# Kernel optimization log

Measured on AMD Instinct MI355X. Metric: run time of the kernel, lower is better.

Reference implementation:

```python
import jax, jax.numpy as jnp
import numpy as np

B, T, H = 32, 512, 1024

def setup_inputs() -> dict:
    key = jax.random.key(0)
    k1, k2, k3, k4, k5 = jax.random.split(key, 5)
    s = 1.0 / np.sqrt(H)  # torch LSTM init scale
    return {
        "x": jax.random.normal(k1, (B, T, H), dtype=jnp.float32),
        "w_ih": jax.random.uniform(k2, (4 * H, H), jnp.float32, -s, s),
        "w_hh": jax.random.uniform(k3, (4 * H, H), jnp.float32, -s, s),
        "b_ih": jax.random.uniform(k4, (4 * H,), jnp.float32, -s, s),
        "b_hh": jax.random.uniform(k5, (4 * H,), jnp.float32, -s, s),
    }

def reference(x, w_ih, w_hh, b_ih, b_hh):
    # Precompute input projections for all steps: [T, B, 4H]
    xg = jnp.einsum('bth,gh->tbg', x, w_ih) + b_ih + b_hh
    h0 = jnp.zeros((x.shape[0], H), x.dtype)
    c0 = jnp.zeros_like(h0)

    def step(carry, xg_t):
        h, c = carry
        gates = xg_t + h @ w_hh.T            # [B, 4H]
        i, f, g, o = jnp.split(gates, 4, axis=-1)  # torch order: i,f,g,o
        i = jax.nn.sigmoid(i)
        f = jax.nn.sigmoid(f)
        g = jnp.tanh(g)
        o = jax.nn.sigmoid(o)
        c = f * c + i * g
        h = o * jnp.tanh(c)
        return (h, c), None

    (h_n, _), _ = jax.lax.scan(step, (h0, c0), xg)
    return h_n  # [B, H] == h_n[0] in torch
```

## Files before the change

### kernel.cpp

```cpp
#include <hip/hip_runtime.h>
#include <cmath>

#define Tn 512
#define Bn 32
#define Hn 1024

typedef short bf16x8 __attribute__((ext_vector_type(8)));
typedef float f32x4 __attribute__((ext_vector_type(4)));

__device__ __forceinline__ unsigned short f2bf_rne(float f) {
    unsigned u = __float_as_uint(f);
    unsigned r = (u + 0x7fffu + ((u >> 16) & 1u)) >> 16;
    return (unsigned short)r;
}
__device__ __forceinline__ float bf2f(unsigned short h) {
    return __uint_as_float((unsigned)h << 16);
}
__device__ __forceinline__ bf16x8 cvt8(float4 a, float4 b) {
    union { unsigned u[4]; bf16x8 v; } o;
    o.u[0] = (unsigned)f2bf_rne(a.x) | ((unsigned)f2bf_rne(a.y) << 16);
    o.u[1] = (unsigned)f2bf_rne(a.z) | ((unsigned)f2bf_rne(a.w) << 16);
    o.u[2] = (unsigned)f2bf_rne(b.x) | ((unsigned)f2bf_rne(b.y) << 16);
    o.u[3] = (unsigned)f2bf_rne(b.z) | ((unsigned)f2bf_rne(b.w) << 16);
    return o.v;
}
__device__ __forceinline__ bf16x8 as_bf8(uint4 u) {
    union { uint4 q; bf16x8 v; } o; o.q = u; return o.v;
}

__device__ __forceinline__ float fsigf(float x) {
    return __builtin_amdgcn_rcpf(1.f + __expf(-x));
}
__device__ __forceinline__ float ftanhf(float x) {
    return 1.f - 2.f * __builtin_amdgcn_rcpf(1.f + __expf(2.f * x));
}

__device__ __forceinline__ void gstore_u32_sc(unsigned* p, unsigned v) {
    asm volatile("global_store_dword %0, %1, off sc0 sc1\n\t"
                 "s_waitcnt vmcnt(0)"
                 :: "v"(p), "v"(v) : "memory");
}
__device__ __forceinline__ void gstore_u32_nd(unsigned* p, unsigned v) {
    asm volatile("global_store_dword %0, %1, off sc0 sc1"
                 :: "v"(p), "v"(v) : "memory");
}
__device__ __forceinline__ unsigned gload_u32_sc(const unsigned* p) {
    unsigned r;
    asm volatile("global_load_dword %0, %1, off sc0 sc1\n\t"
                 "s_waitcnt vmcnt(0)"
                 : "=&v"(r) : "v"(p) : "memory");
    return r;
}
__device__ __forceinline__ void gload_h_sc(const unsigned short* b0,
                                           const unsigned short* b1,
                                           uint4* o0, uint4* o1) {
    asm volatile(
        "global_load_dwordx4 %0, %8, off sc0 sc1\n\t"
        "global_load_dwordx4 %1, %8, off offset:64 sc0 sc1\n\t"
        "global_load_dwordx4 %2, %8, off offset:128 sc0 sc1\n\t"
        "global_load_dwordx4 %3, %8, off offset:192 sc0 sc1\n\t"
        "global_load_dwordx4 %4, %9, off sc0 sc1\n\t"
        "global_load_dwordx4 %5, %9, off offset:64 sc0 sc1\n\t"
        "global_load_dwordx4 %6, %9, off offset:128 sc0 sc1\n\t"
        "global_load_dwordx4 %7, %9, off offset:192 sc0 sc1\n\t"
        "s_waitcnt vmcnt(0)"
        : "=&v"(o0[0]), "=&v"(o0[1]), "=&v"(o0[2]), "=&v"(o0[3]),
          "=&v"(o1[0]), "=&v"(o1[1]), "=&v"(o1[2]), "=&v"(o1[3])
        : "v"(b0), "v"(b1)
        : "memory");
}

__global__ void lstm_flags_init(unsigned* flags) { flags[threadIdx.x] = 0u; }

__global__ __launch_bounds__(512, 2) void lstm_persist_mfma(
    const float* __restrict__ x,
    const float* __restrict__ w_ih,
    const float* __restrict__ w_hh,
    const float* __restrict__ b_ih,
    const float* __restrict__ b_hh,
    unsigned short* __restrict__ hbuf,
    unsigned* __restrict__ flags,
    float* __restrict__ out)
{
    extern __shared__ char smem[];
    unsigned short* lds_w = (unsigned short*)smem;
    float* lds_r = (float*)(smem + 131584);
    unsigned* lds_cnt = (unsigned*)(smem + 131584 + 16384);

    const int tid = threadIdx.x;
    const int bj  = blockIdx.x;
    const int wv  = tid >> 6;
    const int ln  = tid & 63;
    const int l15 = ln & 15;
    const int qd  = ln >> 4;

    if (tid == 0) *lds_cnt = 0u;

    for (int i = 0; i < 16; ++i) {
        int slot = i * 512 + tid;
        int r    = slot >> 9;
        int f4   = slot & 511;
        int n    = (r >> 2) * Hn + bj * 4 + (r & 3);
        float4 v = (f4 < 256) ? ((const float4*)(w_ih + (size_t)n * Hn))[f4]
                              : ((const float4*)(w_hh + (size_t)n * Hn))[f4 - 256];
        unsigned short h0 = f2bf_rne(v.x), h1 = f2bf_rne(v.y);
        unsigned short h2 = f2bf_rne(v.z), h3 = f2bf_rne(v.w);
        unsigned short l0 = f2bf_rne(v.x - bf2f(h0)), l1 = f2bf_rne(v.y - bf2f(h1));
        unsigned short l2 = f2bf_rne(v.z - bf2f(h2)), l3 = f2bf_rne(v.w - bf2f(h3));
        uint2 ph, pl;
        ph.x = (unsigned)h0 | ((unsigned)h1 << 16);
        ph.y = (unsigned)h2 | ((unsigned)h3 << 16);
        pl.x = (unsigned)l0 | ((unsigned)l1 << 16);
        pl.y = (unsigned)l2 | ((unsigned)l3 << 16);
        *(uint2*)(lds_w + (size_t)r        * 2056 + f4 * 4) = ph;
        *(uint2*)(lds_w + (size_t)(r + 16) * 2056 + f4 * 4) = pl;
    }

    float bias0 = 0.f, bias1 = 0.f, bias2 = 0.f, bias3 = 0.f, creg = 0.f;
    if (ln < 16) {
        int col = bj * 4 + (ln & 3);
        bias0 = b_ih[col]          + b_hh[col];
        bias1 = b_ih[Hn + col]     + b_hh[Hn + col];
        bias2 = b_ih[2 * Hn + col] + b_hh[2 * Hn + col];
        bias3 = b_ih[3 * Hn + col] + b_hh[3 * Hn + col];
    }
    __syncthreads();

    const unsigned short* whi_base = lds_w + (size_t)l15 * 2056 + qd * 8;
    const unsigned short* wlo_base = lds_w + (size_t)(l15 + 16) * 2056 + qd * 8;
    const float* xr0 = x + (size_t)l15        * (Tn * Hn) + wv * 128 + qd * 8;
    const float* xr1 = x + (size_t)(16 + l15) * (Tn * Hn) + wv * 128 + qd * 8;
    const size_t hoff0 = (size_t)l15        * Hn + wv * 128 + qd * 8;
    const size_t hoff1 = (size_t)(16 + l15) * Hn + wv * 128 + qd * 8;

    float4 xa0[4], xb0[4], xa1[4], xb1[4];
    #pragma unroll
    for (int j = 0; j < 4; ++j) {
        xa0[j] = *(const float4*)(xr0 + j * 32);
        xb0[j] = *(const float4*)(xr0 + j * 32 + 4);
        xa1[j] = *(const float4*)(xr1 + j * 32);
        xb1[j] = *(const float4*)(xr1 + j * 32 + 4);
    }

    for (int t = 0; t < Tn; ++t) {
        f32x4 a0h = {0.f,0.f,0.f,0.f}, a0l = {0.f,0.f,0.f,0.f};
        f32x4 a1h = {0.f,0.f,0.f,0.f}, a1l = {0.f,0.f,0.f,0.f};

        float4 na0[4], nb0[4], na1[4], nb1[4];
        {
            const int tn = (t + 1 < Tn) ? (t + 1) : t;
            const float* p0 = xr0 + (size_t)tn * Hn;
            const float* p1 = xr1 + (size_t)tn * Hn;
            #pragma unroll
            for (int j = 0; j < 4; ++j) {
                na0[j] = *(const float4*)(p0 + j * 32);
                nb0[j] = *(const float4*)(p0 + j * 32 + 4);
                na1[j] = *(const float4*)(p1 + j * 32);
                nb1[j] = *(const float4*)(p1 + j * 32 + 4);
            }
        }

        #pragma unroll
        for (int j = 0; j < 4; ++j) {
            const int koff = wv * 128 + j * 32;
            bf16x8 ahi = *(const bf16x8*)(whi_base + koff);
            bf16x8 alo = *(const bf16x8*)(wlo_base + koff);
            bf16x8 bf0 = cvt8(xa0[j], xb0[j]);
            bf16x8 bf1 = cvt8(xa1[j], xb1[j]);
            a0h = __builtin_amdgcn_mfma_f32_16x16x32_bf16(ahi, bf0, a0h, 0, 0, 0);
            a0l = __builtin_amdgcn_mfma_f32_16x16x32_bf16(alo, bf0, a0l, 0, 0, 0);
            a1h = __builtin_amdgcn_mfma_f32_16x16x32_bf16(ahi, bf1, a1h, 0, 0, 0);
            a1l = __builtin_amdgcn_mfma_f32_16x16x32_bf16(alo, bf1, a1l, 0, 0, 0);
        }

        if (t > 0) {
            {
                const int src = (ln < 32) ? (wv * 32 + ln) : bj;
                const unsigned* fp = flags + src;
                bool done = false;
                for (;;) {
                    if (!done) done = (gload_u32_sc(fp) >= (unsigned)t);
                    if (__all((int)done)) break;
                }
            }
            const unsigned short* hb = hbuf + (size_t)((t - 1) & 1) * (Bn * Hn);
            uint4 hf0[4], hf1[4];
            gload_h_sc(hb + hoff0, hb + hoff1, hf0, hf1);
            #pragma unroll
            for (int j = 0; j < 4; ++j) {
                const int koff = 1024 + wv * 128 + j * 32;
                bf16x8 ahi = *(const bf16x8*)(whi_base + koff);
                bf16x8 alo = *(const bf16x8*)(wlo_base + koff);
                bf16x8 bf0 = as_bf8(hf0[j]);
                bf16x8 bf1 = as_bf8(hf1[j]);
                a0h = __builtin_amdgcn_mfma_f32_16x16x32_bf16(ahi, bf0, a0h, 0, 0, 0);
                a0l = __builtin_amdgcn_mfma_f32_16x16x32_bf16(alo, bf0, a0l, 0, 0, 0);
                a1h = __builtin_amdgcn_mfma_f32_16x16x32_bf16(ahi, bf1, a1h, 0, 0, 0);
                a1l = __builtin_amdgcn_mfma_f32_16x16x32_bf16(alo, bf1, a1l, 0, 0, 0);
            }
        }

        {
            f32x4 acc0 = a0h + a0l;
            f32x4 acc1 = a1h + a1l;
            float* pr0 = lds_r + (wv * 2 + 0) * 256 + l15;
            float* pr1 = lds_r + (wv * 2 + 1) * 256 + l15;
            #pragma unroll
            for (int r = 0; r < 4; ++r) {
                pr0[(qd * 4 + r) * 16] = acc0[r];
                pr1[(qd * 4 + r) * 16] = acc1[r];
            }
        }
        __syncthreads();

        if (ln < 16) {
            const int e   = (wv << 4) | ln;
            const int b   = e >> 2;
            const int cl  = e & 3;
            const int bt  = b >> 4, c16 = b & 15;
            float s0 = 0.f, s1 = 0.f, s2 = 0.f, s3 = 0.f;
            #pragma unroll
            for (int w8 = 0; w8 < 8; ++w8) {
                const float* base = lds_r + (w8 * 2 + bt) * 256 + c16;
                s0 += base[(0 * 4 + cl) * 16];
                s1 += base[(1 * 4 + cl) * 16];
                s2 += base[(2 * 4 + cl) * 16];
                s3 += base[(3 * 4 + cl) * 16];
            }
            float iv = fsigf(s0 + bias0);
            float fv = fsigf(s1 + bias1);
            float gv = ftanhf(s2 + bias2);
            float ov = fsigf(s3 + bias3);
            creg = fv * creg + iv * gv;
            float hn = ov * ftanhf(creg);
            unsigned short hv = f2bf_rne(hn);
            unsigned up = (unsigned)__shfl_xor((int)(unsigned)hv, 1, 64);
            if (!(ln & 1)) {
                unsigned pack = (unsigned)hv | (up << 16);
                unsigned short* hw = hbuf + (size_t)(t & 1) * (Bn * Hn)
                                   + (size_t)b * Hn + bj * 4 + cl;
                gstore_u32_nd((unsigned*)hw, pack);
            }
            if (t == Tn - 1) out[(size_t)b * Hn + bj * 4 + cl] = hn;
        }
        asm volatile("s_waitcnt vmcnt(0)" ::: "memory");
        if (ln == 0) {
            unsigned old = atomicAdd(lds_cnt, 1u);
            if (old == 8u * (unsigned)t + 7u && (t + 1 < Tn))
                gstore_u32_sc(&flags[bj], (unsigned)(t + 1));
        }

        #pragma unroll
        for (int j = 0; j < 4; ++j) {
            xa0[j] = na0[j]; xb0[j] = nb0[j];
            xa1[j] = na1[j]; xb1[j] = nb1[j];
        }
    }
}

extern "C" void kernel_launch(void* const* d_in, const int* in_sizes, int n_in,
                              void* d_out, int out_size, void* d_ws, size_t ws_size,
                              hipStream_t stream) {
    const float* x    = (const float*)d_in[0];
    const float* w_ih = (const float*)d_in[1];
    const float* w_hh = (const float*)d_in[2];
    const float* b_ih = (const float*)d_in[3];
    const float* b_hh = (const float*)d_in[4];
    float* out = (float*)d_out;

    char* ws = (char*)d_ws;
    unsigned*       flags = (unsigned*)ws;
    unsigned short* hbuf  = (unsigned short*)(ws + 1024);
    (void)in_sizes; (void)n_in; (void)out_size; (void)ws_size;

    const size_t smem_bytes = 131584 + 16384 + 16;

    lstm_flags_init<<<dim3(1), dim3(256), 0, stream>>>(flags);
    lstm_persist_mfma<<<dim3(256), dim3(512), smem_bytes, stream>>>(
        x, w_ih, w_hh, b_ih, b_hh, hbuf, flags, out);
}
```

Before: 3.909 ms.

## Split input projection into chunked GEMM kernel ahead of recurrent persistent kernel

Removes the x·W_ih contribution from the serial recurrent loop and computes it in a separate MFMA GEMM kernel over chunks of 64 timesteps, writing xg to workspace. The persistent kernel now keeps only W_hh in LDS, which halves its LDS footprint, and reads the precomputed gate inputs each step. Cell state is carried across chunk launches through a global cbuf. The cost is 16 extra kernel launches, persistent-kernel restarts that reload weights each chunk, and extra global traffic for xg. The W_ih GEMM is also recomputed per block tile with LDS staging.

Measured after the change: 4.369 ms. +11.8%, slower.

```diff
diff --git a/kernel.cpp b/kernel.cpp
--- a/kernel.cpp
+++ b/kernel.cpp
@@ -4,6 +4,7 @@
 #define Tn 512
 #define Bn 32
 #define Hn 1024
+#define CH 64
 
 typedef short bf16x8 __attribute__((ext_vector_type(8)));
 typedef float f32x4 __attribute__((ext_vector_type(4)));
@@ -72,20 +73,109 @@
 
 __global__ void lstm_flags_init(unsigned* flags) { flags[threadIdx.x] = 0u; }
 
-__global__ __launch_bounds__(512, 2) void lstm_persist_mfma(
+__global__ __launch_bounds__(512, 2) void lstm_xg_gemm(
     const float* __restrict__ x,
     const float* __restrict__ w_ih,
+    float* __restrict__ xg,
+    int t0)
+{
+    extern __shared__ char smem[];
+    unsigned short* lds_a = (unsigned short*)smem;
+
+    const int tid = threadIdx.x;
+    const int gct = blockIdx.x & 31;
+    const int tt  = blockIdx.x >> 5;
+    const int wv  = tid >> 6;
+    const int ln  = tid & 63;
+    const int l15 = ln & 15;
+    const int qd  = ln >> 4;
+    const int tl  = tt * 8 + wv;
+    const int tg  = t0 + tl;
+
+    f32x4 acc[8][2];
+    #pragma unroll
+    for (int gs = 0; gs < 8; ++gs)
+        #pragma unroll
+        for (int h2 = 0; h2 < 2; ++h2)
+            acc[gs][h2] = (f32x4){0.f, 0.f, 0.f, 0.f};
+
+    const float* xrow0 = x + (size_t)l15 * (Tn * Hn) + (size_t)tg * Hn + qd * 8;
+    const float* xrow1 = xrow0 + (size_t)16 * (Tn * Hn);
+
+    for (int kt = 0; kt < 8; ++kt) {
+        #pragma unroll
+        for (int it = 0; it < 8; ++it) {
+            int fi  = it * 512 + tid;
+            int row = fi >> 5;
+            int c   = fi & 31;
+            float4 v = *(const float4*)(w_ih + (size_t)(gct * 128 + row) * Hn
+                                        + kt * 128 + c * 4);
+            unsigned short h0 = f2bf_rne(v.x), h1 = f2bf_rne(v.y);
+            unsigned short h2 = f2bf_rne(v.z), h3 = f2bf_rne(v.w);
+            unsigned short u0 = f2bf_rne(v.x - bf2f(h0)), u1 = f2bf_rne(v.y - bf2f(h1));
+            unsigned short u2 = f2bf_rne(v.z - bf2f(h2)), u3 = f2bf_rne(v.w - bf2f(h3));
+            uint2 ph, pl;
+            ph.x = (unsigned)h0 | ((unsigned)h1 << 16);
+            ph.y = (unsigned)h2 | ((unsigned)h3 << 16);
+            pl.x = (unsigned)u0 | ((unsigned)u1 << 16);
+            pl.y = (unsigned)u2 | ((unsigned)u3 << 16);
+            *(uint2*)(lds_a + (size_t)row * 136 + c * 4) = ph;
+            *(uint2*)(lds_a + (size_t)(row + 128) * 136 + c * 4) = pl;
+        }
+        __syncthreads();
+
+        float4 xv[4][4];
+        #pragma unroll
+        for (int kk = 0; kk < 4; ++kk) {
+            xv[kk][0] = *(const float4*)(xrow0 + kt * 128 + kk * 32);
+            xv[kk][1] = *(const float4*)(xrow0 + kt * 128 + kk * 32 + 4);
+            xv[kk][2] = *(const float4*)(xrow1 + kt * 128 + kk * 32);
+            xv[kk][3] = *(const float4*)(xrow1 + kt * 128 + kk * 32 + 4);
+        }
+        #pragma unroll
+        for (int kk = 0; kk < 4; ++kk) {
+            bf16x8 bf0 = cvt8(xv[kk][0], xv[kk][1]);
+            bf16x8 bf1 = cvt8(xv[kk][2], xv[kk][3]);
+            #pragma unroll
+            for (int gs = 0; gs < 8; ++gs) {
+                bf16x8 ahi = *(const bf16x8*)(lds_a + (size_t)(gs * 16 + l15) * 136
+                                              + kk * 32 + qd * 8);
+                bf16x8 alo = *(const bf16x8*)(lds_a + (size_t)(128 + gs * 16 + l15) * 136
+                                              + kk * 32 + qd * 8);
+                acc[gs][0] = __builtin_amdgcn_mfma_f32_16x16x32_bf16(ahi, bf0, acc[gs][0], 0, 0, 0);
+                acc[gs][0] = __builtin_amdgcn_mfma_f32_16x16x32_bf16(alo, bf0, acc[gs][0], 0, 0, 0);
+                acc[gs][1] = __builtin_amdgcn_mfma_f32_16x16x32_bf16(ahi, bf1, acc[gs][1], 0, 0, 0);
+                acc[gs][1] = __builtin_amdgcn_mfma_f32_16x16x32_bf16(alo, bf1, acc[gs][1], 0, 0, 0);
+            }
+        }
+        __syncthreads();
+    }
+
+    float* xgp = xg + (size_t)tl * (4096 * 32) + (size_t)(gct * 128) * 32 + l15;
+    #pragma unroll
+    for (int gs = 0; gs < 8; ++gs)
+        #pragma unroll
+        for (int h2 = 0; h2 < 2; ++h2)
+            #pragma unroll
+            for (int r = 0; r < 4; ++r)
+                xgp[(size_t)(gs * 16 + qd * 4 + r) * 32 + h2 * 16] = acc[gs][h2][r];
+}
+
+__global__ __launch_bounds__(512, 2) void lstm_persist_mfma(
     const float* __restrict__ w_hh,
     const float* __restrict__ b_ih,
     const float* __restrict__ b_hh,
+    const float* __restrict__ xg,
     unsigned short* __restrict__ hbuf,
+    float* __restrict__ cbuf,
     unsigned* __restrict__ flags,
-    float* __restrict__ out)
+    float* __restrict__ out,
+    int t0)
 {
     extern __shared__ char smem[];
     unsigned short* lds_w = (unsigned short*)smem;
-    float* lds_r = (float*)(smem + 131584);
-    unsigned* lds_cnt = (unsigned*)(smem + 131584 + 16384);
+    float* lds_r = (float*)(smem + 66048);
+    unsigned* lds_cnt = (unsigned*)(smem + 66048 + 18432);
 
     const int tid = threadIdx.x;
     const int bj  = blockIdx.x;
@@ -96,82 +186,58 @@
 
     if (tid == 0) *lds_cnt = 0u;
 
-    for (int i = 0; i < 16; ++i) {
+    for (int i = 0; i < 8; ++i) {
         int slot = i * 512 + tid;
-        int r    = slot >> 9;
-        int f4   = slot & 511;
+        int r    = slot >> 8;
+        int f4   = slot & 255;
         int n    = (r >> 2) * Hn + bj * 4 + (r & 3);
-        float4 v = (f4 < 256) ? ((const float4*)(w_ih + (size_t)n * Hn))[f4]
-                              : ((const float4*)(w_hh + (size_t)n * Hn))[f4 - 256];
+        float4 v = ((const float4*)(w_hh + (size_t)n * Hn))[f4];
         unsigned short h0 = f2bf_rne(v.x), h1 = f2bf_rne(v.y);
         unsigned short h2 = f2bf_rne(v.z), h3 = f2bf_rne(v.w);
-        unsigned short l0 = f2bf_rne(v.x - bf2f(h0)), l1 = f2bf_rne(v.y - bf2f(h1));
-        unsigned short l2 = f2bf_rne(v.z - bf2f(h2)), l3 = f2bf_rne(v.w - bf2f(h3));
+        unsigned short u0 = f2bf_rne(v.x - bf2f(h0)), u1 = f2bf_rne(v.y - bf2f(h1));
+        unsigned short u2 = f2bf_rne(v.z - bf2f(h2)), u3 = f2bf_rne(v.w - bf2f(h3));
         uint2 ph, pl;
         ph.x = (unsigned)h0 | ((unsigned)h1 << 16);
         ph.y = (unsigned)h2 | ((unsigned)h3 << 16);
-        pl.x = (unsigned)l0 | ((unsigned)l1 << 16);
-        pl.y = (unsigned)l2 | ((unsigned)l3 << 16);
-        *(uint2*)(lds_w + (size_t)r        * 2056 + f4 * 4) = ph;
-        *(uint2*)(lds_w + (size_t)(r + 16) * 2056 + f4 * 4) = pl;
+        pl.x = (unsigned)u0 | ((unsigned)u1 << 16);
+        pl.y = (unsigned)u2 | ((unsigned)u3 << 16);
+        *(uint2*)(lds_w + (size_t)r        * 1032 + f4 * 4) = ph;
+        *(uint2*)(lds_w + (size_t)(r + 16) * 1032 + f4 * 4) = pl;
     }
 
     float bias0 = 0.f, bias1 = 0.f, bias2 = 0.f, bias3 = 0.f, creg = 0.f;
+    int fb = 0, fcl = 0;
     if (ln < 16) {
-        int col = bj * 4 + (ln & 3);
+        const int e = (wv << 4) | ln;
+        fb  = e >> 2;
+        fcl = e & 3;
+        int col = bj * 4 + fcl;
         bias0 = b_ih[col]          + b_hh[col];
         bias1 = b_ih[Hn + col]     + b_hh[Hn + col];
         bias2 = b_ih[2 * Hn + col] + b_hh[2 * Hn + col];
         bias3 = b_ih[3 * Hn + col] + b_hh[3 * Hn + col];
+        if (t0 > 0) creg = cbuf[(size_t)fb * Hn + col];
     }
     __syncthreads();
 
-    const unsigned short* whi_base = lds_w + (size_t)l15 * 2056 + qd * 8;
-    const unsigned short* wlo_base = lds_w + (size_t)(l15 + 16) * 2056 + qd * 8;
-    const float* xr0 = x + (size_t)l15        * (Tn * Hn) + wv * 128 + qd * 8;
-    const float* xr1 = x + (size_t)(16 + l15) * (Tn * Hn) + wv * 128 + qd * 8;
+    const unsigned short* whi_base = lds_w + (size_t)l15 * 1032 + qd * 8;
+    const unsigned short* wlo_base = lds_w + (size_t)(l15 + 16) * 1032 + qd * 8;
     const size_t hoff0 = (size_t)l15        * Hn + wv * 128 + qd * 8;
     const size_t hoff1 = (size_t)(16 + l15) * Hn + wv * 128 + qd * 8;
 
-    float4 xa0[4], xb0[4], xa1[4], xb1[4];
-    #pragma unroll
-    for (int j = 0; j < 4; ++j) {
-        xa0[j] = *(const float4*)(xr0 + j * 32);
-        xb0[j] = *(const float4*)(xr0 + j * 32 + 4);
-        xa1[j] = *(const float4*)(xr1 + j * 32);
-        xb1[j] = *(const float4*)(xr1 + j * 32 + 4);
-    }
-
-    for (int t = 0; t < Tn; ++t) {
+    for (int t = t0; t < t0 + CH; ++t) {
+        float xg0 = 0.f, xg1 = 0.f, xg2 = 0.f, xg3 = 0.f;
+        if (ln < 16) {
+            const float* xp = xg + (size_t)(t - t0) * (4096 * 32)
+                            + (size_t)(bj * 4 + fcl) * 32 + fb;
+            xg0 = xp[0];
+            xg1 = xp[1 * 1024 * 32];
+            xg2 = xp[2 * 1024 * 32];
+            xg3 = xp[3 * 1024 * 32];
+        }
+
         f32x4 a0h = {0.f,0.f,0.f,0.f}, a0l = {0.f,0.f,0.f,0.f};
         f32x4 a1h = {0.f,0.f,0.f,0.f}, a1l = {0.f,0.f,0.f,0.f};
-
-        float4 na0[4], nb0[4], na1[4], nb1[4];
-        {
-            const int tn = (t + 1 < Tn) ? (t + 1) : t;
-            const float* p0 = xr0 + (size_t)tn * Hn;
-            const float* p1 = xr1 + (size_t)tn * Hn;
-            #pragma unroll
-            for (int j = 0; j < 4; ++j) {
-                na0[j] = *(const float4*)(p0 + j * 32);
-                nb0[j] = *(const float4*)(p0 + j * 32 + 4);
-                na1[j] = *(const float4*)(p1 + j * 32);
-                nb1[j] = *(const float4*)(p1 + j * 32 + 4);
-            }
-        }
-
-        #pragma unroll
-        for (int j = 0; j < 4; ++j) {
-            const int koff = wv * 128 + j * 32;
-            bf16x8 ahi = *(const bf16x8*)(whi_base + koff);
-            bf16x8 alo = *(const bf16x8*)(wlo_base + koff);
-            bf16x8 bf0 = cvt8(xa0[j], xb0[j]);
-            bf16x8 bf1 = cvt8(xa1[j], xb1[j]);
-            a0h = __builtin_amdgcn_mfma_f32_16x16x32_bf16(ahi, bf0, a0h, 0, 0, 0);
-            a0l = __builtin_amdgcn_mfma_f32_16x16x32_bf16(alo, bf0, a0l, 0, 0, 0);
-            a1h = __builtin_amdgcn_mfma_f32_16x16x32_bf16(ahi, bf1, a1h, 0, 0, 0);
-            a1l = __builtin_amdgcn_mfma_f32_16x16x32_bf16(alo, bf1, a1l, 0, 0, 0);
-        }
 
         if (t > 0) {
             {
@@ -188,7 +254,7 @@
             gload_h_sc(hb + hoff0, hb + hoff1, hf0, hf1);
             #pragma unroll
             for (int j = 0; j < 4; ++j) {
-                const int koff = 1024 + wv * 128 + j * 32;
+                const int koff = wv * 128 + j * 32;
                 bf16x8 ahi = *(const bf16x8*)(whi_base + koff);
                 bf16x8 alo = *(const bf16x8*)(wlo_base + koff);
                 bf16x8 bf0 = as_bf8(hf0[j]);
@@ -203,34 +269,31 @@
         {
             f32x4 acc0 = a0h + a0l;
             f32x4 acc1 = a1h + a1l;
-            float* pr0 = lds_r + (wv * 2 + 0) * 256 + l15;
-            float* pr1 = lds_r + (wv * 2 + 1) * 256 + l15;
+            float* pr0 = lds_r + (wv * 2 + 0) * 288 + l15;
+            float* pr1 = lds_r + (wv * 2 + 1) * 288 + l15;
             #pragma unroll
             for (int r = 0; r < 4; ++r) {
-                pr0[(qd * 4 + r) * 16] = acc0[r];
-                pr1[(qd * 4 + r) * 16] = acc1[r];
+                pr0[(qd * 4 + r) * 18] = acc0[r];
+                pr1[(qd * 4 + r) * 18] = acc1[r];
             }
         }
         __syncthreads();
 
         if (ln < 16) {
-            const int e   = (wv << 4) | ln;
-            const int b   = e >> 2;
-            const int cl  = e & 3;
-            const int bt  = b >> 4, c16 = b & 15;
+            const int bt = fb >> 4, c16 = fb & 15;
             float s0 = 0.f, s1 = 0.f, s2 = 0.f, s3 = 0.f;
             #pragma unroll
             for (int w8 = 0; w8 < 8; ++w8) {
-                const float* base = lds_r + (w8 * 2 + bt) * 256 + c16;
-                s0 += base[(0 * 4 + cl) * 16];
-                s1 += base[(1 * 4 + cl) * 16];
-                s2 += base[(2 * 4 + cl) * 16];
-                s3 += base[(3 * 4 + cl) * 16];
-            }
-            float iv = fsigf(s0 + bias0);
-            float fv = fsigf(s1 + bias1);
-            float gv = ftanhf(s2 + bias2);
-            float ov = fsigf(s3 + bias3);
+                const float* base = lds_r + (w8 * 2 + bt) * 288 + c16;
+                s0 += base[(0 * 4 + fcl) * 18];
+                s1 += base[(1 * 4 + fcl) * 18];
+                s2 += base[(2 * 4 + fcl) * 18];
+                s3 += base[(3 * 4 + fcl) * 18];
+            }
+            float iv = fsigf(s0 + xg0 + bias0);
+            float fv = fsigf(s1 + xg1 + bias1);
+            float gv = ftanhf(s2 + xg2 + bias2);
+            float ov = fsigf(s3 + xg3 + bias3);
             creg = fv * creg + iv * gv;
             float hn = ov * ftanhf(creg);
             unsigned short hv = f2bf_rne(hn);
@@ -238,22 +301,18 @@
             if (!(ln & 1)) {
                 unsigned pack = (unsigned)hv | (up << 16);
                 unsigned short* hw = hbuf + (size_t)(t & 1) * (Bn * Hn)
-                                   + (size_t)b * Hn + bj * 4 + cl;
+                                   + (size_t)fb * Hn + bj * 4 + fcl;
                 gstore_u32_nd((unsigned*)hw, pack);
             }
-            if (t == Tn - 1) out[(size_t)b * Hn + bj * 4 + cl] = hn;
+            if (t == Tn - 1) out[(size_t)fb * Hn + bj * 4 + fcl] = hn;
+            if (t == t0 + CH - 1) cbuf[(size_t)fb * Hn + bj * 4 + fcl] = creg;
         }
         asm volatile("s_waitcnt vmcnt(0)" ::: "memory");
         if (ln == 0) {
+            unsigned lt = (unsigned)(t - t0);
             unsigned old = atomicAdd(lds_cnt, 1u);
-            if (old == 8u * (unsigned)t + 7u && (t + 1 < Tn))
+            if (old == 8u * lt + 7u && (t + 1 < Tn))
                 gstore_u32_sc(&flags[bj], (unsigned)(t + 1));
-        }
-
-        #pragma unroll
-        for (int j = 0; j < 4; ++j) {
-            xa0[j] = na0[j]; xb0[j] = nb0[j];
-            xa1[j] = na1[j]; xb1[j] = nb1[j];
         }
     }
 }
@@ -271,11 +330,18 @@
     char* ws = (char*)d_ws;
     unsigned*       flags = (unsigned*)ws;
     unsigned short* hbuf  = (unsigned short*)(ws + 1024);
+    float*          cbuf  = (float*)(ws + 1024 + 131072);
+    float*          xg    = (float*)(ws + 1024 + 131072 + 131072);
     (void)in_sizes; (void)n_in; (void)out_size; (void)ws_size;
 
-    const size_t smem_bytes = 131584 + 16384 + 16;
+    const size_t smem_a = 256 * 136 * 2;
+    const size_t smem_b = 66048 + 18432 + 16;
 
     lstm_flags_init<<<dim3(1), dim3(256), 0, stream>>>(flags);
-    lstm_persist_mfma<<<dim3(256), dim3(512), smem_bytes, stream>>>(
-        x, w_ih, w_hh, b_ih, b_hh, hbuf, flags, out);
-}
+    for (int c = 0; c < Tn / CH; ++c) {
+        lstm_xg_gemm<<<dim3(256), dim3(512), smem_a, stream>>>(
+            x, w_ih, xg, c * CH);
+        lstm_persist_mfma<<<dim3(256), dim3(512), smem_b, stream>>>(
+            w_hh, b_ih, b_hh, xg, hbuf, cbuf, flags, out, c * CH);
+    }
+}
```

## Restructure persistent LSTM into thin 2-wave blocks with per-half sync flags

Applied to the files above, without the earlier changes.

Each block now runs 2 waves instead of 8. Each wave owns 16 batch rows and covers the full K=1024 on its own, which removes the LDS cross-wave reduction and the __syncthreads on every step. The high part of W_hh is kept in registers, and the input projection for step t+1 runs after publishing h, so it overlaps with the wait. Flags are split per half and polled with vectorized min-of-4 loads plus s_sleep, and h is stored as 64-bit packs. In exchange, each wave now does serial per-step MFMA work over the whole K, and register pressure is very high with 32 bf16x8 weight registers plus 32 uint4 h loads.

Measured after the change: 10.78 ms. 176% more time.

```diff
diff --git a/kernel.cpp b/kernel.cpp
--- a/kernel.cpp
+++ b/kernel.cpp
@@ -40,39 +40,43 @@
                  "s_waitcnt vmcnt(0)"
                  :: "v"(p), "v"(v) : "memory");
 }
-__device__ __forceinline__ void gstore_u32_nd(unsigned* p, unsigned v) {
-    asm volatile("global_store_dword %0, %1, off sc0 sc1"
+__device__ __forceinline__ void gstore_u64_nd(unsigned long long* p,
+                                              unsigned long long v) {
+    asm volatile("global_store_dwordx2 %0, %1, off sc0 sc1"
                  :: "v"(p), "v"(v) : "memory");
 }
-__device__ __forceinline__ unsigned gload_u32_sc(const unsigned* p) {
-    unsigned r;
-    asm volatile("global_load_dword %0, %1, off sc0 sc1\n\t"
+__device__ __forceinline__ uint4 gload_u4_sc(const unsigned* p) {
+    uint4 r;
+    asm volatile("global_load_dwordx4 %0, %1, off sc0 sc1\n\t"
                  "s_waitcnt vmcnt(0)"
                  : "=&v"(r) : "v"(p) : "memory");
     return r;
 }
-__device__ __forceinline__ void gload_h_sc(const unsigned short* b0,
-                                           const unsigned short* b1,
-                                           uint4* o0, uint4* o1) {
+__device__ __forceinline__ void gload8_nd(const unsigned short* b, uint4* o) {
     asm volatile(
         "global_load_dwordx4 %0, %8, off sc0 sc1\n\t"
         "global_load_dwordx4 %1, %8, off offset:64 sc0 sc1\n\t"
         "global_load_dwordx4 %2, %8, off offset:128 sc0 sc1\n\t"
         "global_load_dwordx4 %3, %8, off offset:192 sc0 sc1\n\t"
-        "global_load_dwordx4 %4, %9, off sc0 sc1\n\t"
-        "global_load_dwordx4 %5, %9, off offset:64 sc0 sc1\n\t"
-        "global_load_dwordx4 %6, %9, off offset:128 sc0 sc1\n\t"
-        "global_load_dwordx4 %7, %9, off offset:192 sc0 sc1\n\t"
-        "s_waitcnt vmcnt(0)"
-        : "=&v"(o0[0]), "=&v"(o0[1]), "=&v"(o0[2]), "=&v"(o0[3]),
-          "=&v"(o1[0]), "=&v"(o1[1]), "=&v"(o1[2]), "=&v"(o1[3])
-        : "v"(b0), "v"(b1)
+        "global_load_dwordx4 %4, %8, off offset:256 sc0 sc1\n\t"
+        "global_load_dwordx4 %5, %8, off offset:320 sc0 sc1\n\t"
+        "global_load_dwordx4 %6, %8, off offset:384 sc0 sc1\n\t"
+        "global_load_dwordx4 %7, %8, off offset:448 sc0 sc1"
+        : "=&v"(o[0]), "=&v"(o[1]), "=&v"(o[2]), "=&v"(o[3]),
+          "=&v"(o[4]), "=&v"(o[5]), "=&v"(o[6]), "=&v"(o[7])
+        : "v"(b)
         : "memory");
 }
 
+__device__ __forceinline__ unsigned min4u(uint4 f) {
+    unsigned a = f.x < f.y ? f.x : f.y;
+    unsigned b = f.z < f.w ? f.z : f.w;
+    return a < b ? a : b;
+}
+
 __global__ void lstm_flags_init(unsigned* flags) { flags[threadIdx.x] = 0u; }
 
-__global__ __launch_bounds__(512, 2) void lstm_persist_mfma(
+__global__ __launch_bounds__(128, 1) void lstm_persist_thin(
     const float* __restrict__ x,
     const float* __restrict__ w_ih,
     const float* __restrict__ w_hh,
@@ -84,176 +88,164 @@
 {
     extern __shared__ char smem[];
     unsigned short* lds_w = (unsigned short*)smem;
-    float* lds_r = (float*)(smem + 131584);
-    unsigned* lds_cnt = (unsigned*)(smem + 131584 + 16384);
-
-    const int tid = threadIdx.x;
-    const int bj  = blockIdx.x;
-    const int wv  = tid >> 6;
-    const int ln  = tid & 63;
-    const int l15 = ln & 15;
-    const int qd  = ln >> 4;
-
-    if (tid == 0) *lds_cnt = 0u;
-
-    for (int i = 0; i < 16; ++i) {
-        int slot = i * 512 + tid;
-        int r    = slot >> 9;
-        int f4   = slot & 511;
-        int n    = (r >> 2) * Hn + bj * 4 + (r & 3);
-        float4 v = (f4 < 256) ? ((const float4*)(w_ih + (size_t)n * Hn))[f4]
-                              : ((const float4*)(w_hh + (size_t)n * Hn))[f4 - 256];
+
+    const int tid  = threadIdx.x;
+    const int bj   = blockIdx.x;
+    const int half = tid >> 6;
+    const int ln   = tid & 63;
+    const int l15  = ln & 15;
+    const int qd   = ln >> 4;
+
+    for (int i = 0; i < 64; ++i) {
+        int slot = i * 128 + tid;
+        int m    = slot >> 12;
+        int rr   = (slot >> 8) & 15;
+        int f4   = slot & 255;
+        const float* W = m ? w_hh : w_ih;
+        int n = (rr >> 2) * Hn + bj * 4 + (rr & 3);
+        float4 v = ((const float4*)(W + (size_t)n * Hn))[f4];
         unsigned short h0 = f2bf_rne(v.x), h1 = f2bf_rne(v.y);
         unsigned short h2 = f2bf_rne(v.z), h3 = f2bf_rne(v.w);
-        unsigned short l0 = f2bf_rne(v.x - bf2f(h0)), l1 = f2bf_rne(v.y - bf2f(h1));
-        unsigned short l2 = f2bf_rne(v.z - bf2f(h2)), l3 = f2bf_rne(v.w - bf2f(h3));
+        unsigned short u0 = f2bf_rne(v.x - bf2f(h0)), u1 = f2bf_rne(v.y - bf2f(h1));
+        unsigned short u2 = f2bf_rne(v.z - bf2f(h2)), u3 = f2bf_rne(v.w - bf2f(h3));
         uint2 ph, pl;
         ph.x = (unsigned)h0 | ((unsigned)h1 << 16);
         ph.y = (unsigned)h2 | ((unsigned)h3 << 16);
-        pl.x = (unsigned)l0 | ((unsigned)l1 << 16);
-        pl.y = (unsigned)l2 | ((unsigned)l3 << 16);
-        *(uint2*)(lds_w + (size_t)r        * 2056 + f4 * 4) = ph;
-        *(uint2*)(lds_w + (size_t)(r + 16) * 2056 + f4 * 4) = pl;
+        pl.x = (unsigned)u0 | ((unsigned)u1 << 16);
+        pl.y = (unsigned)u2 | ((unsigned)u3 << 16);
+        unsigned short* base = lds_w + (size_t)m * 33024;
+        *(uint2*)(base + (size_t)rr        * 1032 + f4 * 4) = ph;
+        *(uint2*)(base + (size_t)(rr + 16) * 1032 + f4 * 4) = pl;
     }
 
-    float bias0 = 0.f, bias1 = 0.f, bias2 = 0.f, bias3 = 0.f, creg = 0.f;
-    if (ln < 16) {
-        int col = bj * 4 + (ln & 3);
-        bias0 = b_ih[col]          + b_hh[col];
-        bias1 = b_ih[Hn + col]     + b_hh[Hn + col];
-        bias2 = b_ih[2 * Hn + col] + b_hh[2 * Hn + col];
-        bias3 = b_ih[3 * Hn + col] + b_hh[3 * Hn + col];
+    float bias[4];
+    {
+        int col = bj * 4 + qd;
+        #pragma unroll
+        for (int g = 0; g < 4; ++g)
+            bias[g] = b_ih[g * Hn + col] + b_hh[g * Hn + col];
     }
     __syncthreads();
 
-    const unsigned short* whi_base = lds_w + (size_t)l15 * 2056 + qd * 8;
-    const unsigned short* wlo_base = lds_w + (size_t)(l15 + 16) * 2056 + qd * 8;
-    const float* xr0 = x + (size_t)l15        * (Tn * Hn) + wv * 128 + qd * 8;
-    const float* xr1 = x + (size_t)(16 + l15) * (Tn * Hn) + wv * 128 + qd * 8;
-    const size_t hoff0 = (size_t)l15        * Hn + wv * 128 + qd * 8;
-    const size_t hoff1 = (size_t)(16 + l15) * Hn + wv * 128 + qd * 8;
-
-    float4 xa0[4], xb0[4], xa1[4], xb1[4];
+    const unsigned short* Axh = lds_w + (size_t)l15 * 1032 + qd * 8;
+    const unsigned short* Axl = Axh + (size_t)16 * 1032;
+    const unsigned short* Ahh = Axh + 33024;
+    const unsigned short* Ahl = Axl + 33024;
+    const float* xlane = x + (size_t)(half * 16 + l15) * (Tn * Hn) + qd * 8;
+    const size_t hlane = (size_t)(half * 16 + l15) * Hn + qd * 8;
+
+    bf16x8 whh[32];
     #pragma unroll
-    for (int j = 0; j < 4; ++j) {
-        xa0[j] = *(const float4*)(xr0 + j * 32);
-        xb0[j] = *(const float4*)(xr0 + j * 32 + 4);
-        xa1[j] = *(const float4*)(xr1 + j * 32);
-        xb1[j] = *(const float4*)(xr1 + j * 32 + 4);
-    }
+    for (int j = 0; j < 32; ++j)
+        whh[j] = *(const bf16x8*)(Ahh + j * 32);
+
+    f32x4 c0 = {0,0,0,0}, c1 = {0,0,0,0}, c2 = {0,0,0,0}, c3 = {0,0,0,0};
+    float creg = 0.f;
+
+    auto xphase = [&](int tt) {
+        const float* xp = xlane + (size_t)tt * Hn;
+        #pragma unroll
+        for (int jb = 0; jb < 4; ++jb) {
+            float4 va[8], vb[8];
+            #pragma unroll
+            for (int jj = 0; jj < 8; ++jj) {
+                va[jj] = *(const float4*)(xp + (jb * 8 + jj) * 32);
+                vb[jj] = *(const float4*)(xp + (jb * 8 + jj) * 32 + 4);
+            }
+            #pragma unroll
+            for (int jj = 0; jj < 8; ++jj) {
+                const int j = jb * 8 + jj;
+                bf16x8 xb  = cvt8(va[jj], vb[jj]);
+                bf16x8 ahi = *(const bf16x8*)(Axh + j * 32);
+                bf16x8 alo = *(const bf16x8*)(Axl + j * 32);
+                if (j & 1) {
+                    c2 = __builtin_amdgcn_mfma_f32_16x16x32_bf16(ahi, xb, c2, 0, 0, 0);
+                    c3 = __builtin_amdgcn_mfma_f32_16x16x32_bf16(alo, xb, c3, 0, 0, 0);
+                } else {
+                    c0 = __builtin_amdgcn_mfma_f32_16x16x32_bf16(ahi, xb, c0, 0, 0, 0);
+                    c1 = __builtin_amdgcn_mfma_f32_16x16x32_bf16(alo, xb, c1, 0, 0, 0);
+                }
+            }
+        }
+    };
+
+    xphase(0);
 
     for (int t = 0; t < Tn; ++t) {
-        f32x4 a0h = {0.f,0.f,0.f,0.f}, a0l = {0.f,0.f,0.f,0.f};
-        f32x4 a1h = {0.f,0.f,0.f,0.f}, a1l = {0.f,0.f,0.f,0.f};
-
-        float4 na0[4], nb0[4], na1[4], nb1[4];
-        {
-            const int tn = (t + 1 < Tn) ? (t + 1) : t;
-            const float* p0 = xr0 + (size_t)tn * Hn;
-            const float* p1 = xr1 + (size_t)tn * Hn;
-            #pragma unroll
-            for (int j = 0; j < 4; ++j) {
-                na0[j] = *(const float4*)(p0 + j * 32);
-                nb0[j] = *(const float4*)(p0 + j * 32 + 4);
-                na1[j] = *(const float4*)(p1 + j * 32);
-                nb1[j] = *(const float4*)(p1 + j * 32 + 4);
-            }
-        }
-
-        #pragma unroll
-        for (int j = 0; j < 4; ++j) {
-            const int koff = wv * 128 + j * 32;
-            bf16x8 ahi = *(const bf16x8*)(whi_base + koff);
-            bf16x8 alo = *(const bf16x8*)(wlo_base + koff);
-            bf16x8 bf0 = cvt8(xa0[j], xb0[j]);
-            bf16x8 bf1 = cvt8(xa1[j], xb1[j]);
-            a0h = __builtin_amdgcn_mfma_f32_16x16x32_bf16(ahi, bf0, a0h, 0, 0, 0);
-            a0l = __builtin_amdgcn_mfma_f32_16x16x32_bf16(alo, bf0, a0l, 0, 0, 0);
-            a1h = __builtin_amdgcn_mfma_f32_16x16x32_bf16(ahi, bf1, a1h, 0, 0, 0);
-            a1l = __builtin_amdgcn_mfma_f32_16x16x32_bf16(alo, bf1, a1l, 0, 0, 0);
-        }
-
         if (t > 0) {
             {
-                const int src = (ln < 32) ? (wv * 32 + ln) : bj;
-                const unsigned* fp = flags + src;
-                bool done = false;
-                for (;;) {
-                    if (!done) done = (gload_u32_sc(fp) >= (unsigned)t);
-                    if (__all((int)done)) break;
+                const unsigned* fp = flags + half * 256 + ln * 4;
+                bool done = (min4u(gload_u4_sc(fp)) >= (unsigned)t);
+                while (!__all((int)done)) {
+                    __builtin_amdgcn_s_sleep(2);
+                    if (!done)
+                        done = (min4u(gload_u4_sc(fp)) >= (unsigned)t);
                 }
             }
-            const unsigned short* hb = hbuf + (size_t)((t - 1) & 1) * (Bn * Hn);
-            uint4 hf0[4], hf1[4];
-            gload_h_sc(hb + hoff0, hb + hoff1, hf0, hf1);
-            #pragma unroll
-            for (int j = 0; j < 4; ++j) {
-                const int koff = 1024 + wv * 128 + j * 32;
-                bf16x8 ahi = *(const bf16x8*)(whi_base + koff);
-                bf16x8 alo = *(const bf16x8*)(wlo_base + koff);
-                bf16x8 bf0 = as_bf8(hf0[j]);
-                bf16x8 bf1 = as_bf8(hf1[j]);
-                a0h = __builtin_amdgcn_mfma_f32_16x16x32_bf16(ahi, bf0, a0h, 0, 0, 0);
-                a0l = __builtin_amdgcn_mfma_f32_16x16x32_bf16(alo, bf0, a0l, 0, 0, 0);
-                a1h = __builtin_amdgcn_mfma_f32_16x16x32_bf16(ahi, bf1, a1h, 0, 0, 0);
-                a1l = __builtin_amdgcn_mfma_f32_16x16x32_bf16(alo, bf1, a1l, 0, 0, 0);
-            }
-        }
-
-        {
-            f32x4 acc0 = a0h + a0l;
-            f32x4 acc1 = a1h + a1l;
-            float* pr0 = lds_r + (wv * 2 + 0) * 256 + l15;
-            float* pr1 = lds_r + (wv * 2 + 1) * 256 + l15;
+            const unsigned short* hb =
+                hbuf + (size_t)((t - 1) & 1) * (Bn * Hn) + hlane;
+            uint4 hf[32];
+            gload8_nd(hb,       &hf[0]);
+            gload8_nd(hb + 256, &hf[8]);
+            gload8_nd(hb + 512, &hf[16]);
+            gload8_nd(hb + 768, &hf[24]);
+            asm volatile("s_waitcnt vmcnt(0)" ::: "memory");
+            __builtin_amdgcn_sched_barrier(0);
+
+            #pragma unroll
+            for (int j = 0; j < 32; ++j) {
+                bf16x8 hbf = as_bf8(hf[j]);
+                bf16x8 alo = *(const bf16x8*)(Ahl + j * 32);
+                if (j & 1) {
+                    c2 = __builtin_amdgcn_mfma_f32_16x16x32_bf16(whh[j], hbf, c2, 0, 0, 0);
+                    c3 = __builtin_amdgcn_mfma_f32_16x16x32_bf16(alo,    hbf, c3, 0, 0, 0);
+                } else {
+                    c0 = __builtin_amdgcn_mfma_f32_16x16x32_bf16(whh[j], hbf, c0, 0, 0, 0);
+                    c1 = __builtin_amdgcn_mfma_f32_16x16x32_bf16(alo,    hbf, c1, 0, 0, 0);
+                }
+            }
+        }
+
+        f32x4 s = (c0 + c1) + (c2 + c3);
+        float g4[4];
+        #pragma unroll
+        for (int g = 0; g < 4; ++g) {
             #pragma unroll
             for (int r = 0; r < 4; ++r) {
-                pr0[(qd * 4 + r) * 16] = acc0[r];
-                pr1[(qd * 4 + r) * 16] = acc1[r];
-            }
-        }
-        __syncthreads();
-
-        if (ln < 16) {
-            const int e   = (wv << 4) | ln;
-            const int b   = e >> 2;
-            const int cl  = e & 3;
-            const int bt  = b >> 4, c16 = b & 15;
-            float s0 = 0.f, s1 = 0.f, s2 = 0.f, s3 = 0.f;
-            #pragma unroll
-            for (int w8 = 0; w8 < 8; ++w8) {
-                const float* base = lds_r + (w8 * 2 + bt) * 256 + c16;
-                s0 += base[(0 * 4 + cl) * 16];
-                s1 += base[(1 * 4 + cl) * 16];
-                s2 += base[(2 * 4 + cl) * 16];
-                s3 += base[(3 * 4 + cl) * 16];
-            }
-            float iv = fsigf(s0 + bias0);
-            float fv = fsigf(s1 + bias1);
-            float gv = ftanhf(s2 + bias2);
-            float ov = fsigf(s3 + bias3);
-            creg = fv * creg + iv * gv;
-            float hn = ov * ftanhf(creg);
-            unsigned short hv = f2bf_rne(hn);
-            unsigned up = (unsigned)__shfl_xor((int)(unsigned)hv, 1, 64);
-            if (!(ln & 1)) {
-                unsigned pack = (unsigned)hv | (up << 16);
-                unsigned short* hw = hbuf + (size_t)(t & 1) * (Bn * Hn)
-                                   + (size_t)b * Hn + bj * 4 + cl;
-                gstore_u32_nd((unsigned*)hw, pack);
-            }
-            if (t == Tn - 1) out[(size_t)b * Hn + bj * 4 + cl] = hn;
+                float tmp = __shfl(s[r], g * 16 + l15, 64);
+                if (qd == r) g4[g] = tmp;
+            }
+        }
+
+        float iv = fsigf(g4[0] + bias[0]);
+        float fv = fsigf(g4[1] + bias[1]);
+        float gv = ftanhf(g4[2] + bias[2]);
+        float ov = fsigf(g4[3] + bias[3]);
+        creg = fv * creg + iv * gv;
+        float hn = ov * ftanhf(creg);
+
+        unsigned hv  = (unsigned)f2bf_rne(hn);
+        unsigned hv1 = (unsigned)__shfl((int)hv, l15 + 16, 64);
+        unsigned hv2 = (unsigned)__shfl((int)hv, l15 + 32, 64);
+        unsigned hv3 = (unsigned)__shfl((int)hv, l15 + 48, 64);
+        if (qd == 0) {
+            unsigned long long pk =
+                ((unsigned long long)(hv2 | (hv3 << 16)) << 32) |
+                (unsigned long long)(hv | (hv1 << 16));
+            unsigned short* hw = hbuf + (size_t)(t & 1) * (Bn * Hn)
+                               + (size_t)(half * 16 + l15) * Hn + bj * 4;
+            gstore_u64_nd((unsigned long long*)hw, pk);
         }
         asm volatile("s_waitcnt vmcnt(0)" ::: "memory");
-        if (ln == 0) {
-            unsigned old = atomicAdd(lds_cnt, 1u);
-            if (old == 8u * (unsigned)t + 7u && (t + 1 < Tn))
-                gstore_u32_sc(&flags[bj], (unsigned)(t + 1));
-        }
-
-        #pragma unroll
-        for (int j = 0; j < 4; ++j) {
-            xa0[j] = na0[j]; xb0[j] = nb0[j];
-            xa1[j] = na1[j]; xb1[j] = nb1[j];
+        if (ln == 0 && t + 1 < Tn)
+            gstore_u32_sc(flags + half * 256 + bj, (unsigned)(t + 1));
+        if (t == Tn - 1)
+            out[(size_t)(half * 16 + l15) * Hn + bj * 4 + qd] = hn;
+
+        if (t + 1 < Tn) {
+            c0 = (f32x4){0,0,0,0}; c1 = (f32x4){0,0,0,0};
+            c2 = (f32x4){0,0,0,0}; c3 = (f32x4){0,0,0,0};
+            xphase(t + 1);
         }
     }
 }
@@ -270,12 +262,12 @@
 
     char* ws = (char*)d_ws;
     unsigned*       flags = (unsigned*)ws;
-    unsigned short* hbuf  = (unsigned short*)(ws + 1024);
+    unsigned short* hbuf  = (unsigned short*)(ws + 2048);
     (void)in_sizes; (void)n_in; (void)out_size; (void)ws_size;
 
-    const size_t smem_bytes = 131584 + 16384 + 16;
-
-    lstm_flags_init<<<dim3(1), dim3(256), 0, stream>>>(flags);
-    lstm_persist_mfma<<<dim3(256), dim3(512), smem_bytes, stream>>>(
+    const size_t smem_bytes = 2 * 33024 * 2;
+
+    lstm_flags_init<<<dim3(1), dim3(512), 0, stream>>>(flags);
+    lstm_persist_thin<<<dim3(256), dim3(128), smem_bytes, stream>>>(
         x, w_ih, w_hh, b_ih, b_hh, hbuf, flags, out);
 }
```

## Replace per-block flag polling with rotating global atomic counters and pad LDS reduction

Applied to the files above, without the earlier changes.

Before, each wave polled 32 per-block flags with uncached loads. Now one wave polls a single global counter, chosen from 8 rotating slots indexed by step, until all 256 blocks have atomically incremented it, then releases the block with a barrier. This cuts the flag traffic per step and adds s_sleep backoff while polling, at the cost of contention on a single atomic location and an extra block barrier. The LDS reduction buffer is also padded (stride 18 instead of 16) to reduce bank conflicts.

Result: slower. 4.158 ms (+6.4%).

```diff
diff --git a/kernel.cpp b/kernel.cpp
--- a/kernel.cpp
+++ b/kernel.cpp
@@ -35,11 +35,6 @@
     return 1.f - 2.f * __builtin_amdgcn_rcpf(1.f + __expf(2.f * x));
 }
 
-__device__ __forceinline__ void gstore_u32_sc(unsigned* p, unsigned v) {
-    asm volatile("global_store_dword %0, %1, off sc0 sc1\n\t"
-                 "s_waitcnt vmcnt(0)"
-                 :: "v"(p), "v"(v) : "memory");
-}
 __device__ __forceinline__ void gstore_u32_nd(unsigned* p, unsigned v) {
     asm volatile("global_store_dword %0, %1, off sc0 sc1"
                  :: "v"(p), "v"(v) : "memory");
@@ -70,7 +65,7 @@
         : "memory");
 }
 
-__global__ void lstm_flags_init(unsigned* flags) { flags[threadIdx.x] = 0u; }
+__global__ void lstm_flags_init(unsigned* cnt) { cnt[threadIdx.x] = 0u; }
 
 __global__ __launch_bounds__(512, 2) void lstm_persist_mfma(
     const float* __restrict__ x,
@@ -79,13 +74,13 @@
     const float* __restrict__ b_ih,
     const float* __restrict__ b_hh,
     unsigned short* __restrict__ hbuf,
-    unsigned* __restrict__ flags,
+    unsigned* __restrict__ cnt,
     float* __restrict__ out)
 {
     extern __shared__ char smem[];
     unsigned short* lds_w = (unsigned short*)smem;
     float* lds_r = (float*)(smem + 131584);
-    unsigned* lds_cnt = (unsigned*)(smem + 131584 + 16384);
+    unsigned* lds_cnt = (unsigned*)(smem + 131584 + 18432);
 
     const int tid = threadIdx.x;
     const int bj  = blockIdx.x;
@@ -117,8 +112,12 @@
     }
 
     float bias0 = 0.f, bias1 = 0.f, bias2 = 0.f, bias3 = 0.f, creg = 0.f;
+    int fb = 0, fcl = 0;
     if (ln < 16) {
-        int col = bj * 4 + (ln & 3);
+        const int e = (wv << 4) | ln;
+        fb  = e >> 2;
+        fcl = e & 3;
+        int col = bj * 4 + fcl;
         bias0 = b_ih[col]          + b_hh[col];
         bias1 = b_ih[Hn + col]     + b_hh[Hn + col];
         bias2 = b_ih[2 * Hn + col] + b_hh[2 * Hn + col];
@@ -174,15 +173,14 @@
         }
 
         if (t > 0) {
-            {
-                const int src = (ln < 32) ? (wv * 32 + ln) : bj;
-                const unsigned* fp = flags + src;
-                bool done = false;
-                for (;;) {
-                    if (!done) done = (gload_u32_sc(fp) >= (unsigned)t);
-                    if (__all((int)done)) break;
-                }
-            }
+            if (wv == 0) {
+                const unsigned thr = 256u * (((unsigned)(t - 1) >> 3) + 1u);
+                const unsigned* cp = cnt + ((t - 1) & 7) * 16;
+                while (gload_u32_sc(cp) < thr)
+                    __builtin_amdgcn_s_sleep(1);
+            }
+            __syncthreads();
+
             const unsigned short* hb = hbuf + (size_t)((t - 1) & 1) * (Bn * Hn);
             uint4 hf0[4], hf1[4];
             gload_h_sc(hb + hoff0, hb + hoff1, hf0, hf1);
@@ -203,29 +201,26 @@
         {
             f32x4 acc0 = a0h + a0l;
             f32x4 acc1 = a1h + a1l;
-            float* pr0 = lds_r + (wv * 2 + 0) * 256 + l15;
-            float* pr1 = lds_r + (wv * 2 + 1) * 256 + l15;
+            float* pr0 = lds_r + (wv * 2 + 0) * 288 + l15;
+            float* pr1 = lds_r + (wv * 2 + 1) * 288 + l15;
             #pragma unroll
             for (int r = 0; r < 4; ++r) {
-                pr0[(qd * 4 + r) * 16] = acc0[r];
-                pr1[(qd * 4 + r) * 16] = acc1[r];
+                pr0[(qd * 4 + r) * 18] = acc0[r];
+                pr1[(qd * 4 + r) * 18] = acc1[r];
             }
         }
         __syncthreads();
 
         if (ln < 16) {
-            const int e   = (wv << 4) | ln;
-            const int b   = e >> 2;
-            const int cl  = e & 3;
-            const int bt  = b >> 4, c16 = b & 15;
+            const int bt = fb >> 4, c16 = fb & 15;
             float s0 = 0.f, s1 = 0.f, s2 = 0.f, s3 = 0.f;
             #pragma unroll
             for (int w8 = 0; w8 < 8; ++w8) {
-                const float* base = lds_r + (w8 * 2 + bt) * 256 + c16;
-                s0 += base[(0 * 4 + cl) * 16];
-                s1 += base[(1 * 4 + cl) * 16];
-                s2 += base[(2 * 4 + cl) * 16];
-                s3 += base[(3 * 4 + cl) * 16];
+                const float* base = lds_r + (w8 * 2 + bt) * 288 + c16;
+                s0 += base[(0 * 4 + fcl) * 18];
+                s1 += base[(1 * 4 + fcl) * 18];
+                s2 += base[(2 * 4 + fcl) * 18];
+                s3 += base[(3 * 4 + fcl) * 18];
             }
             float iv = fsigf(s0 + bias0);
             float fv = fsigf(s1 + bias1);
@@ -238,16 +233,16 @@
             if (!(ln & 1)) {
                 unsigned pack = (unsigned)hv | (up << 16);
                 unsigned short* hw = hbuf + (size_t)(t & 1) * (Bn * Hn)
-                                   + (size_t)b * Hn + bj * 4 + cl;
+                                   + (size_t)fb * Hn + bj * 4 + fcl;
                 gstore_u32_nd((unsigned*)hw, pack);
             }
-            if (t == Tn - 1) out[(size_t)b * Hn + bj * 4 + cl] = hn;
+            if (t == Tn - 1) out[(size_t)fb * Hn + bj * 4 + fcl] = hn;
         }
         asm volatile("s_waitcnt vmcnt(0)" ::: "memory");
         if (ln == 0) {
             unsigned old = atomicAdd(lds_cnt, 1u);
             if (old == 8u * (unsigned)t + 7u && (t + 1 < Tn))
-                gstore_u32_sc(&flags[bj], (unsigned)(t + 1));
+                atomicAdd(cnt + (t & 7) * 16, 1u);
         }
 
         #pragma unroll
@@ -269,13 +264,13 @@
     float* out = (float*)d_out;
 
     char* ws = (char*)d_ws;
-    unsigned*       flags = (unsigned*)ws;
-    unsigned short* hbuf  = (unsigned short*)(ws + 1024);
+    unsigned*       cnt  = (unsigned*)ws;
+    unsigned short* hbuf = (unsigned short*)(ws + 1024);
     (void)in_sizes; (void)n_in; (void)out_size; (void)ws_size;
 
-    const size_t smem_bytes = 131584 + 16384 + 16;
-
-    lstm_flags_init<<<dim3(1), dim3(256), 0, stream>>>(flags);
+    const size_t smem_bytes = 131584 + 18432 + 16;
+
+    lstm_flags_init<<<dim3(1), dim3(256), 0, stream>>>(cnt);
     lstm_persist_mfma<<<dim3(256), dim3(512), smem_bytes, stream>>>(
-        x, w_ih, w_hh, b_ih, b_hh, hbuf, flags, out);
-}
+        x, w_ih, w_hh, b_ih, b_hh, hbuf, cnt, out);
+}
```
